# Kernel tuning notes

Hardware: AMD Instinct MI355X
Metric: run time of the kernel (lower is better)

Reference implementation:

```python
import jax, jax.numpy as jnp
import numpy as np

N = 100000
E = 1600000
IN_C = 128
HID = 32
H1 = 4
OUT_C = 32
H2 = 1
NEG_SLOPE = 0.2


def setup_inputs() -> dict:
    key = jax.random.key(0)
    ks = jax.random.split(key, 12)
    g = 0.1  # glorot-ish scale
    return {
        "x": jax.random.normal(ks[0], (N, IN_C), jnp.float32),
        "edge_index": jax.random.randint(ks[1], (2, E), 0, N, jnp.int64),
        "W1": jax.random.normal(ks[2], (IN_C, H1 * HID), jnp.float32) * g,
        "att_src1": jax.random.normal(ks[3], (H1, HID), jnp.float32) * g,
        "att_dst1": jax.random.normal(ks[4], (H1, HID), jnp.float32) * g,
        "b1": jnp.zeros((H1 * HID,), jnp.float32),
        "W2": jax.random.normal(ks[5], (H1 * HID, H2 * OUT_C), jnp.float32) * g,
        "att_src2": jax.random.normal(ks[6], (H2, OUT_C), jnp.float32) * g,
        "att_dst2": jax.random.normal(ks[7], (H2, OUT_C), jnp.float32) * g,
        "b2": jnp.zeros((H2 * OUT_C,), jnp.float32),
    }


def gat_conv(x, src, dst, W, att_src, att_dst, bias, heads, ch):
    n = x.shape[0]
    h = (x @ W).reshape(n, heads, ch)                      # [N,H,C]
    a_src = jnp.sum(h * att_src, axis=-1)                  # [N,H]
    a_dst = jnp.sum(h * att_dst, axis=-1)                  # [N,H]
    e = jax.nn.leaky_relu(a_src[src] + a_dst[dst], NEG_SLOPE)  # [E,H]
    # segment softmax over destination neighborhoods
    m = jax.ops.segment_max(e, dst, num_segments=n)        # [N,H]
    ex = jnp.exp(e - m[dst])
    denom = jax.ops.segment_sum(ex, dst, num_segments=n)   # [N,H]
    alpha = ex / (denom[dst] + 1e-16)                      # [E,H]
    msg = h[src] * alpha[:, :, None]                       # [E,H,C]
    out = jax.ops.segment_sum(msg, dst, num_segments=n)    # [N,H,C]
    return out.reshape(n, heads * ch) + bias


def reference(x, edge_index, W1, att_src1, att_dst1, b1, W2, att_src2, att_dst2, b2):
    # PyG GATConv add_self_loops=True
    loops = jnp.arange(N, dtype=edge_index.dtype)
    src = jnp.concatenate([edge_index[0], loops])
    dst = jnp.concatenate([edge_index[1], loops])
    # dropout is a no-op at inference
    h = gat_conv(x, src, dst, W1, att_src1, att_dst1, b1, H1, HID)
    h = jax.nn.relu(h)
    out = gat_conv(h, src, dst, W2, att_src2, att_dst2, b2, H2, OUT_C)
    return out
```

## Files before the change

### kernel.cpp

```cpp
#include <hip/hip_runtime.h>
#include <hip/hip_bf16.h>


#define NSLOPE 0.2f
#define GSTRIDE 136
#define NB_MAX 400
#define CHUNK 4096
#define CAP 5632

typedef __attribute__((ext_vector_type(8))) short short8;
typedef __attribute__((ext_vector_type(4))) float floatx4;

__device__ __forceinline__ float leaky(float v) { return v > 0.f ? v : NSLOPE * v; }

__device__ __forceinline__ unsigned short f2bf(float f) {
  __hip_bfloat16 b = __float2bfloat16(f);
  return *reinterpret_cast<unsigned short*>(&b);
}
__device__ __forceinline__ float bf2f(unsigned int u) {
  return __uint_as_float(u << 16);
}
__device__ __forceinline__ unsigned int pack2(float a, float b) {
  return (unsigned int)f2bf(a) | ((unsigned int)f2bf(b) << 16);
}

__global__ __launch_bounds__(256) void zero_kernel(int* __restrict__ bincur, int nb) {
  int i = blockIdx.x * 256 + threadIdx.x;
  if (i < nb) bincur[i] = i * CAP;
}

__global__ __launch_bounds__(256) void binA_kernel(const int* __restrict__ ei,
                                                   int* __restrict__ bincur,
                                                   unsigned int* __restrict__ staging,
                                                   int E, int ET, int nb) {
  __shared__ int hist[NB_MAX];
  __shared__ int run[NB_MAX];
  __shared__ int rbase[NB_MAX];
  const int t = threadIdx.x;
  const int base = blockIdx.x * CHUNK;
  for (int i = t; i < nb; i += 256) { hist[i] = 0; run[i] = 0; }
  __syncthreads();
  int se[16], de[16];
#pragma unroll
  for (int j = 0; j < 16; j++) {
    int idx = base + j * 256 + t;
    if (idx < ET) {
      if (idx < E) { se[j] = ei[idx]; de[j] = ei[E + idx]; }
      else         { se[j] = de[j] = idx - E; }
      atomicAdd(&hist[de[j] >> 8], 1);
    } else de[j] = -1;
  }
  __syncthreads();
  for (int i = t; i < nb; i += 256)
    rbase[i] = hist[i] ? atomicAdd(&bincur[i], hist[i]) : 0;
  __syncthreads();
#pragma unroll
  for (int j = 0; j < 16; j++) {
    if (de[j] >= 0) {
      int b = de[j] >> 8;
      int ofs = atomicAdd(&run[b], 1);
      staging[(size_t)rbase[b] + ofs] =
          (unsigned)se[j] | ((unsigned)(de[j] & 255) << 17);
    }
  }
}

__global__ __launch_bounds__(256) void binB_kernel(const unsigned int* __restrict__ staging,
                                                   const int* __restrict__ bincur,
                                                   int* __restrict__ rowbeg,
                                                   int* __restrict__ rowend,
                                                   int* __restrict__ bucket, int n) {
  __shared__ int cnt[256];
  __shared__ int cur[256];
  const int b = blockIdx.x;
  const int t = threadIdx.x;
  const int d0 = b << 8;
  const int nd = min(256, n - d0);
  const int base = b * CAP;
  const int rcnt = bincur[b] - base;
  cnt[t] = 0;
  __syncthreads();
  for (int j = t; j < rcnt; j += 256) {
    unsigned int r = staging[(size_t)base + j];
    atomicAdd(&cnt[r >> 17], 1);
  }
  __syncthreads();
  int v = cnt[t];
  cur[t] = v;
  __syncthreads();
  for (int off = 1; off < 256; off <<= 1) {
    int add = (t >= off) ? cur[t - off] : 0;
    __syncthreads();
    cur[t] += add;
    __syncthreads();
  }
  int start = base + cur[t] - v;
  if (t < nd) { rowbeg[d0 + t] = start; rowend[d0 + t] = start + v; }
  __syncthreads();
  cur[t] = start;
  __syncthreads();
  for (int j = t; j < rcnt; j += 256) {
    unsigned int r = staging[(size_t)base + j];
    int pos = atomicAdd(&cur[r >> 17], 1);
    bucket[pos] = (int)(r & 0x1FFFFu);
  }
}

__global__ __launch_bounds__(256, 2) void gemm1_kernel(const float* __restrict__ x,
                                                       const float* __restrict__ W,
                                                       const float* __restrict__ atts,
                                                       const float* __restrict__ attd,
                                                       unsigned short* __restrict__ h,
                                                       float* __restrict__ asrc,
                                                       float* __restrict__ adst, int n) {
  __shared__ __align__(16) unsigned short xs[128 * GSTRIDE];
  __shared__ __align__(16) unsigned short wt[128 * GSTRIDE];
  __shared__ float att_s[128], att_d[128];
  const int tid = threadIdx.x;
  const int row0 = blockIdx.x * 128;

  if (tid < 128) { att_s[tid] = atts[tid]; att_d[tid] = attd[tid]; }

  const float4* w4 = (const float4*)W;
#pragma unroll
  for (int i = 0; i < 16; i++) {
    int idx = tid + i * 256;
    int k = idx >> 5, n0 = (idx & 31) * 4;
    float4 v = w4[idx];
    float vv[4] = {v.x, v.y, v.z, v.w};
#pragma unroll
    for (int jj = 0; jj < 4; jj++) {
      int j = (jj + tid) & 3;
      wt[(n0 + j) * GSTRIDE + k] = f2bf(vv[j]);
    }
  }

  const float4* x4 = (const float4*)x;
#pragma unroll
  for (int i = 0; i < 16; i++) {
    int idx = tid + i * 256;
    int r = idx >> 5, c4 = idx & 31;
    float4 v = make_float4(0.f, 0.f, 0.f, 0.f);
    if (row0 + r < n) v = x4[(size_t)(row0 + r) * 32 + c4];
    unsigned int* p = (unsigned int*)&xs[r * GSTRIDE + c4 * 4];
    p[0] = pack2(v.x, v.y);
    p[1] = pack2(v.z, v.w);
  }
  __syncthreads();

  const int l = tid & 63;
  const int w = tid >> 6;
  const int mrow = l & 15;
  const int q = l >> 4;
  floatx4 acc[2][8];
#pragma unroll
  for (int mt = 0; mt < 2; mt++)
#pragma unroll
    for (int nt = 0; nt < 8; nt++) acc[mt][nt] = (floatx4){0.f, 0.f, 0.f, 0.f};

#pragma unroll
  for (int ks = 0; ks < 4; ks++) {
    const int k0 = ks * 32 + q * 8;
    short8 a0 = *(const short8*)&xs[(w * 32 + mrow) * GSTRIDE + k0];
    short8 a1 = *(const short8*)&xs[(w * 32 + 16 + mrow) * GSTRIDE + k0];
#pragma unroll
    for (int nt = 0; nt < 8; nt++) {
      short8 b = *(const short8*)&wt[(nt * 16 + mrow) * GSTRIDE + k0];
      acc[0][nt] = __builtin_amdgcn_mfma_f32_16x16x32_bf16(a0, b, acc[0][nt], 0, 0, 0);
      acc[1][nt] = __builtin_amdgcn_mfma_f32_16x16x32_bf16(a1, b, acc[1][nt], 0, 0, 0);
    }
  }
  __syncthreads();

#pragma unroll
  for (int mt = 0; mt < 2; mt++)
#pragma unroll
    for (int nt = 0; nt < 8; nt++)
#pragma unroll
      for (int i = 0; i < 4; i++) {
        int r = w * 32 + mt * 16 + q * 4 + i;
        xs[r * GSTRIDE + nt * 16 + mrow] = f2bf(acc[mt][nt][i]);
      }
  __syncthreads();

#pragma unroll
  for (int i = 0; i < 8; i++) {
    int idx = tid + i * 256;
    int r = idx >> 4, c8 = (idx & 15) * 8;
    if (row0 + r < n) {
      unsigned int* p = (unsigned int*)&xs[r * GSTRIDE + c8];
      uint4 v = make_uint4(p[0], p[1], p[2], p[3]);
      *(uint4*)(h + (size_t)(row0 + r) * 128 + c8) = v;
    }
  }

#pragma unroll
  for (int rr = 0; rr < 2; rr++) {
    int row = (tid >> 2) + rr * 64;
    int head = tid & 3;
    float ss = 0.f, sd = 0.f;
#pragma unroll
    for (int c = 0; c < 32; c++) {
      int cr = (c + tid) & 31;
      float hv = bf2f(xs[row * GSTRIDE + head * 32 + cr]);
      ss += hv * att_s[head * 32 + cr];
      sd += hv * att_d[head * 32 + cr];
    }
    if (row0 + row < n) {
      asrc[(size_t)(row0 + row) * 4 + head] = ss;
      adst[(size_t)(row0 + row) * 4 + head] = sd;
    }
  }
}

__global__ __launch_bounds__(256, 2) void gemm2_kernel(const float* __restrict__ agg1,
                                                       const float* __restrict__ b1,
                                                       const float* __restrict__ W,
                                                       const float* __restrict__ atts,
                                                       const float* __restrict__ attd,
                                                       unsigned short* __restrict__ h2,
                                                       float* __restrict__ asrc,
                                                       float* __restrict__ adst, int n) {
  __shared__ __align__(16) unsigned short xs[128 * GSTRIDE];
  __shared__ __align__(16) unsigned short wt[32 * GSTRIDE];
  __shared__ __align__(16) unsigned short hs[128 * 36];
  __shared__ float att_s[32], att_d[32];
  const int tid = threadIdx.x;
  const int row0 = blockIdx.x * 128;

  if (tid < 32) { att_s[tid] = atts[tid]; att_d[tid] = attd[tid]; }

  const float4* w4 = (const float4*)W;
#pragma unroll
  for (int i = 0; i < 4; i++) {
    int idx = tid + i * 256;
    int k = idx >> 3, n0 = (idx & 7) * 4;
    float4 v = w4[idx];
    float vv[4] = {v.x, v.y, v.z, v.w};
#pragma unroll
    for (int jj = 0; jj < 4; jj++) {
      int j = (jj + tid) & 3;
      wt[(n0 + j) * GSTRIDE + k] = f2bf(vv[j]);
    }
  }

  const float4* a4 = (const float4*)agg1;
#pragma unroll
  for (int i = 0; i < 16; i++) {
    int idx = tid + i * 256;
    int r = idx >> 5, c4 = idx & 31;
    float4 v = make_float4(0.f, 0.f, 0.f, 0.f);
    if (row0 + r < n) {
      float4 a = a4[(size_t)(row0 + r) * 32 + c4];
      float4 b = ((const float4*)b1)[c4];
      v.x = fmaxf(a.x + b.x, 0.f);
      v.y = fmaxf(a.y + b.y, 0.f);
      v.z = fmaxf(a.z + b.z, 0.f);
      v.w = fmaxf(a.w + b.w, 0.f);
    }
    unsigned int* p = (unsigned int*)&xs[r * GSTRIDE + c4 * 4];
    p[0] = pack2(v.x, v.y);
    p[1] = pack2(v.z, v.w);
  }
  __syncthreads();

  const int l = tid & 63;
  const int w = tid >> 6;
  const int mrow = l & 15;
  const int q = l >> 4;
  floatx4 acc[2][2];
#pragma unroll
  for (int mt = 0; mt < 2; mt++)
#pragma unroll
    for (int nt = 0; nt < 2; nt++) acc[mt][nt] = (floatx4){0.f, 0.f, 0.f, 0.f};

#pragma unroll
  for (int ks = 0; ks < 4; ks++) {
    const int k0 = ks * 32 + q * 8;
    short8 a0 = *(const short8*)&xs[(w * 32 + mrow) * GSTRIDE + k0];
    short8 a1 = *(const short8*)&xs[(w * 32 + 16 + mrow) * GSTRIDE + k0];
#pragma unroll
    for (int nt = 0; nt < 2; nt++) {
      short8 b = *(const short8*)&wt[(nt * 16 + mrow) * GSTRIDE + k0];
      acc[0][nt] = __builtin_amdgcn_mfma_f32_16x16x32_bf16(a0, b, acc[0][nt], 0, 0, 0);
      acc[1][nt] = __builtin_amdgcn_mfma_f32_16x16x32_bf16(a1, b, acc[1][nt], 0, 0, 0);
    }
  }

#pragma unroll
  for (int mt = 0; mt < 2; mt++)
#pragma unroll
    for (int nt = 0; nt < 2; nt++)
#pragma unroll
      for (int i = 0; i < 4; i++) {
        int r = w * 32 + mt * 16 + q * 4 + i;
        hs[r * 36 + nt * 16 + mrow] = f2bf(acc[mt][nt][i]);
      }
  __syncthreads();

#pragma unroll
  for (int i = 0; i < 4; i++) {
    int idx = tid + i * 256;
    int r = idx >> 3, c4 = (idx & 7) * 4;
    if (row0 + r < n) {
      unsigned int* p = (unsigned int*)&hs[r * 36 + c4];
      *(uint2*)(h2 + (size_t)(row0 + r) * 32 + c4) = make_uint2(p[0], p[1]);
    }
  }

  if (tid < 128) {
    int row = tid;
    float ss = 0.f, sd = 0.f;
#pragma unroll
    for (int c = 0; c < 32; c++) {
      int cr = (c + tid) & 31;
      float hv = bf2f(hs[row * 36 + cr]);
      ss += hv * att_s[cr];
      sd += hv * att_d[cr];
    }
    if (row0 + row < n) { asrc[row0 + row] = ss; adst[row0 + row] = sd; }
  }
}

__global__ __launch_bounds__(256) void g1_kernel(const int* __restrict__ rowbeg,
                                                 const int* __restrict__ rowend,
                                                 const int* __restrict__ bucket,
                                                 const float* __restrict__ asrc,
                                                 const float* __restrict__ adst,
                                                 const unsigned int* __restrict__ h,
                                                 float* __restrict__ agg, int n) {
  const int lane = threadIdx.x & 63;
  const int g = lane >> 3;
  const int l8 = lane & 7;
  const int head = l8 >> 1;
  const int d = blockIdx.x * 4 + (threadIdx.x >> 6);
  if (d >= n) return;
  const float ad = adst[(size_t)d * 4 + head];
  const int beg = rowbeg[d], end = rowend[d];
  float num[16];
#pragma unroll
  for (int j = 0; j < 16; j++) num[j] = 0.f;
  float den = 0.f;

  int i = beg + g;
  if (i < end) {
    int s = bucket[i];
    for (;;) {
      float a = asrc[(size_t)s * 4 + head];
      const uint4* hp = (const uint4*)(h + (size_t)s * 64 + l8 * 8);
      uint4 h0 = hp[0];
      uint4 h1v = hp[1];
      int i2 = i + 8;
      int s2 = (i2 < end) ? bucket[i2] : 0;
      float w = __expf(leaky(a + ad));
      den += w;
      num[0]  += w * bf2f(h0.x & 0xffffu);  num[1]  += w * bf2f(h0.x >> 16);
      num[2]  += w * bf2f(h0.y & 0xffffu);  num[3]  += w * bf2f(h0.y >> 16);
      num[4]  += w * bf2f(h0.z & 0xffffu);  num[5]  += w * bf2f(h0.z >> 16);
      num[6]  += w * bf2f(h0.w & 0xffffu);  num[7]  += w * bf2f(h0.w >> 16);
      num[8]  += w * bf2f(h1v.x & 0xffffu); num[9]  += w * bf2f(h1v.x >> 16);
      num[10] += w * bf2f(h1v.y & 0xffffu); num[11] += w * bf2f(h1v.y >> 16);
      num[12] += w * bf2f(h1v.z & 0xffffu); num[13] += w * bf2f(h1v.z >> 16);
      num[14] += w * bf2f(h1v.w & 0xffffu); num[15] += w * bf2f(h1v.w >> 16);
      if (i2 >= end) break;
      i = i2; s = s2;
    }
  }
#pragma unroll
  for (int j = 0; j < 16; j++) {
    num[j] += __shfl_xor(num[j], 8, 64);
    num[j] += __shfl_xor(num[j], 16, 64);
    num[j] += __shfl_xor(num[j], 32, 64);
  }
  den += __shfl_xor(den, 8, 64);
  den += __shfl_xor(den, 16, 64);
  den += __shfl_xor(den, 32, 64);
  if (g == 0) {
    float inv = 1.f / (den + 1e-16f);
    float* p = agg + (size_t)d * 128 + l8 * 16;
#pragma unroll
    for (int j = 0; j < 4; j++)
      *(float4*)(p + j * 4) = make_float4(num[j * 4] * inv, num[j * 4 + 1] * inv,
                                          num[j * 4 + 2] * inv, num[j * 4 + 3] * inv);
  }
}

__global__ __launch_bounds__(256) void g2_kernel(const int* __restrict__ rowbeg,
                                                 const int* __restrict__ rowend,
                                                 const int* __restrict__ bucket,
                                                 const float* __restrict__ asrc,
                                                 const float* __restrict__ adst,
                                                 const unsigned int* __restrict__ h2,
                                                 const float* __restrict__ b2,
                                                 float* __restrict__ out, int n) {
  const int lane = threadIdx.x & 63;
  const int g = lane >> 3;
  const int l8 = lane & 7;
  const int d = blockIdx.x * 4 + (threadIdx.x >> 6);
  if (d >= n) return;
  const float ad = adst[d];
  const int beg = rowbeg[d], end = rowend[d];
  float num[4];
#pragma unroll
  for (int j = 0; j < 4; j++) num[j] = 0.f;
  float den = 0.f;

  int i = beg + g;
  if (i < end) {
    int s = bucket[i];
    for (;;) {
      float a = asrc[s];
      uint2 hv = *(const uint2*)(h2 + (size_t)s * 16 + l8 * 2);
      int i2 = i + 8;
      int s2 = (i2 < end) ? bucket[i2] : 0;
      float w = __expf(leaky(a + ad));
      den += w;
      num[0] += w * bf2f(hv.x & 0xffffu); num[1] += w * bf2f(hv.x >> 16);
      num[2] += w * bf2f(hv.y & 0xffffu); num[3] += w * bf2f(hv.y >> 16);
      if (i2 >= end) break;
      i = i2; s = s2;
    }
  }
#pragma unroll
  for (int j = 0; j < 4; j++) {
    num[j] += __shfl_xor(num[j], 8, 64);
    num[j] += __shfl_xor(num[j], 16, 64);
    num[j] += __shfl_xor(num[j], 32, 64);
  }
  den += __shfl_xor(den, 8, 64);
  den += __shfl_xor(den, 16, 64);
  den += __shfl_xor(den, 32, 64);
  if (g == 0) {
    float inv = 1.f / (den + 1e-16f);
    float4 bv = ((const float4*)b2)[l8];
    *(float4*)(out + (size_t)d * 32 + l8 * 4) =
        make_float4(num[0] * inv + bv.x, num[1] * inv + bv.y,
                    num[2] * inv + bv.z, num[3] * inv + bv.w);
  }
}

extern "C" void kernel_launch(void* const* d_in, const int* in_sizes, int n_in,
                              void* d_out, int out_size, void* d_ws, size_t ws_size,
                              hipStream_t stream) {
  const float* x = (const float*)d_in[0];
  const int* ei = (const int*)d_in[1];
  const float* W1 = (const float*)d_in[2];
  const float* atts1 = (const float*)d_in[3];
  const float* attd1 = (const float*)d_in[4];
  const float* b1 = (const float*)d_in[5];
  const float* W2 = (const float*)d_in[6];
  const float* atts2 = (const float*)d_in[7];
  const float* attd2 = (const float*)d_in[8];
  const float* b2 = (const float*)d_in[9];
  float* out = (float*)d_out;

  const int N = in_sizes[0] / 128;
  const int E = in_sizes[1] / 2;
  const int ET = E + N;
  const int NB = (N + 255) >> 8;
  const int NCH = (ET + CHUNK - 1) / CHUNK;

  float* wsf = (float*)d_ws;
  float* agg1 = wsf;
  float* asrc1 = agg1 + (size_t)N * 128;
  float* adst1 = asrc1 + (size_t)N * 4;
  float* asrc2 = adst1 + (size_t)N * 4;
  float* adst2 = asrc2 + (size_t)N;
  unsigned short* h1 = (unsigned short*)(adst2 + (size_t)N);
  unsigned short* h2 = h1;
  int* rowbeg = (int*)(h1 + (size_t)N * 128);
  int* rowend = rowbeg + N;
  int* bucket = rowend + N;
  int* bincur = bucket + (size_t)NB * CAP;
  unsigned int* staging = (unsigned int*)(bincur + NB);

  zero_kernel<<<(NB + 255) / 256, 256, 0, stream>>>(bincur, NB);
  gemm1_kernel<<<(N + 127) / 128, 256, 0, stream>>>(x, W1, atts1, attd1, h1, asrc1, adst1, N);
  binA_kernel<<<NCH, 256, 0, stream>>>(ei, bincur, staging, E, ET, NB);
  binB_kernel<<<NB, 256, 0, stream>>>(staging, bincur, rowbeg, rowend, bucket, N);
  g1_kernel<<<(N + 3) / 4, 256, 0, stream>>>(rowbeg, rowend, bucket, asrc1, adst1,
                                             (const unsigned int*)h1, agg1, N);
  gemm2_kernel<<<(N + 127) / 128, 256, 0, stream>>>(agg1, b1, W2, atts2, attd2, h2, asrc2, adst2, N);
  g2_kernel<<<(N + 3) / 4, 256, 0, stream>>>(rowbeg, rowend, bucket, asrc2, adst2,
                                             (const unsigned int*)h2, b2, out, N);
}
```

Measured before the change: 306.2 us.

## Fuse binning into GEMM1 launch and CSR build into aggregation kernels via LDS

GEMM1 and the edge-binning pass now run in one launch, with blocks split by role, so the two independent phases can overlap. The second binning pass (local sort per 256-node bin) is folded into both aggregation kernels: each 1024-thread block rebuilds its bin's CSR in LDS, so the global bucket, rowbeg and rowend arrays are no longer written and reread. The layer-1 aggregate is stored as bf16 instead of fp32, halving that intermediate's traffic into GEMM2. In exchange the local sort is done twice, occupancy may drop from large LDS and block sizes, and the extra bf16 rounding slightly reduces precision.

```diff
diff --git a/kernel.cpp b/kernel.cpp
--- a/kernel.cpp
+++ b/kernel.cpp
@@ -29,191 +29,254 @@
   if (i < nb) bincur[i] = i * CAP;
 }
 
-__global__ __launch_bounds__(256) void binA_kernel(const int* __restrict__ ei,
-                                                   int* __restrict__ bincur,
-                                                   unsigned int* __restrict__ staging,
-                                                   int E, int ET, int nb) {
-  __shared__ int hist[NB_MAX];
-  __shared__ int run[NB_MAX];
-  __shared__ int rbase[NB_MAX];
-  const int t = threadIdx.x;
-  const int base = blockIdx.x * CHUNK;
-  for (int i = t; i < nb; i += 256) { hist[i] = 0; run[i] = 0; }
-  __syncthreads();
-  int se[16], de[16];
-#pragma unroll
-  for (int j = 0; j < 16; j++) {
-    int idx = base + j * 256 + t;
-    if (idx < ET) {
-      if (idx < E) { se[j] = ei[idx]; de[j] = ei[E + idx]; }
-      else         { se[j] = de[j] = idx - E; }
-      atomicAdd(&hist[de[j] >> 8], 1);
-    } else de[j] = -1;
-  }
-  __syncthreads();
-  for (int i = t; i < nb; i += 256)
-    rbase[i] = hist[i] ? atomicAdd(&bincur[i], hist[i]) : 0;
-  __syncthreads();
-#pragma unroll
-  for (int j = 0; j < 16; j++) {
-    if (de[j] >= 0) {
-      int b = de[j] >> 8;
-      int ofs = atomicAdd(&run[b], 1);
-      staging[(size_t)rbase[b] + ofs] =
-          (unsigned)se[j] | ((unsigned)(de[j] & 255) << 17);
-    }
-  }
-}
-
-__global__ __launch_bounds__(256) void binB_kernel(const unsigned int* __restrict__ staging,
-                                                   const int* __restrict__ bincur,
-                                                   int* __restrict__ rowbeg,
-                                                   int* __restrict__ rowend,
-                                                   int* __restrict__ bucket, int n) {
-  __shared__ int cnt[256];
-  __shared__ int cur[256];
+__global__ __launch_bounds__(256, 2) void fused1_kernel(
+    const float* __restrict__ x, const float* __restrict__ W,
+    const float* __restrict__ atts, const float* __restrict__ attd,
+    unsigned short* __restrict__ h, float* __restrict__ asrc, float* __restrict__ adst,
+    int n, int g1blocks,
+    const int* __restrict__ ei, int* __restrict__ bincur,
+    unsigned int* __restrict__ staging, int E, int ET, int nb) {
+  __shared__ __align__(16) unsigned char smem[70656];
+  const int tid = threadIdx.x;
+
+  if (blockIdx.x < g1blocks) {
+    unsigned short* xs = (unsigned short*)smem;
+    unsigned short* wt = (unsigned short*)(smem + 34816);
+    float* att_s = (float*)(smem + 69632);
+    float* att_d = (float*)(smem + 70144);
+    const int row0 = blockIdx.x * 128;
+
+    if (tid < 128) { att_s[tid] = atts[tid]; att_d[tid] = attd[tid]; }
+
+    const float4* w4 = (const float4*)W;
+#pragma unroll
+    for (int i = 0; i < 16; i++) {
+      int idx = tid + i * 256;
+      int k = idx >> 5, n0 = (idx & 31) * 4;
+      float4 v = w4[idx];
+      float vv[4] = {v.x, v.y, v.z, v.w};
+#pragma unroll
+      for (int jj = 0; jj < 4; jj++) {
+        int j = (jj + tid) & 3;
+        wt[(n0 + j) * GSTRIDE + k] = f2bf(vv[j]);
+      }
+    }
+
+    const float4* x4 = (const float4*)x;
+#pragma unroll
+    for (int i = 0; i < 16; i++) {
+      int idx = tid + i * 256;
+      int r = idx >> 5, c4 = idx & 31;
+      float4 v = make_float4(0.f, 0.f, 0.f, 0.f);
+      if (row0 + r < n) v = x4[(size_t)(row0 + r) * 32 + c4];
+      unsigned int* p = (unsigned int*)&xs[r * GSTRIDE + c4 * 4];
+      p[0] = pack2(v.x, v.y);
+      p[1] = pack2(v.z, v.w);
+    }
+    __syncthreads();
+
+    const int l = tid & 63;
+    const int w = tid >> 6;
+    const int mrow = l & 15;
+    const int q = l >> 4;
+    floatx4 acc[2][8];
+#pragma unroll
+    for (int mt = 0; mt < 2; mt++)
+#pragma unroll
+      for (int nt = 0; nt < 8; nt++) acc[mt][nt] = (floatx4){0.f, 0.f, 0.f, 0.f};
+
+#pragma unroll
+    for (int ks = 0; ks < 4; ks++) {
+      const int k0 = ks * 32 + q * 8;
+      short8 a0 = *(const short8*)&xs[(w * 32 + mrow) * GSTRIDE + k0];
+      short8 a1 = *(const short8*)&xs[(w * 32 + 16 + mrow) * GSTRIDE + k0];
+#pragma unroll
+      for (int nt = 0; nt < 8; nt++) {
+        short8 b = *(const short8*)&wt[(nt * 16 + mrow) * GSTRIDE + k0];
+        acc[0][nt] = __builtin_amdgcn_mfma_f32_16x16x32_bf16(a0, b, acc[0][nt], 0, 0, 0);
+        acc[1][nt] = __builtin_amdgcn_mfma_f32_16x16x32_bf16(a1, b, acc[1][nt], 0, 0, 0);
+      }
+    }
+    __syncthreads();
+
+#pragma unroll
+    for (int mt = 0; mt < 2; mt++)
+#pragma unroll
+      for (int nt = 0; nt < 8; nt++)
+#pragma unroll
+        for (int i = 0; i < 4; i++) {
+          int r = w * 32 + mt * 16 + q * 4 + i;
+          xs[r * GSTRIDE + nt * 16 + mrow] = f2bf(acc[mt][nt][i]);
+        }
+    __syncthreads();
+
+#pragma unroll
+    for (int i = 0; i < 8; i++) {
+      int idx = tid + i * 256;
+      int r = idx >> 4, c8 = (idx & 15) * 8;
+      if (row0 + r < n) {
+        unsigned int* p = (unsigned int*)&xs[r * GSTRIDE + c8];
+        uint4 v = make_uint4(p[0], p[1], p[2], p[3]);
+        *(uint4*)(h + (size_t)(row0 + r) * 128 + c8) = v;
+      }
+    }
+
+#pragma unroll
+    for (int rr = 0; rr < 2; rr++) {
+      int row = (tid >> 2) + rr * 64;
+      int head = tid & 3;
+      float ss = 0.f, sd = 0.f;
+#pragma unroll
+      for (int c = 0; c < 32; c++) {
+        int cr = (c + tid) & 31;
+        float hv = bf2f(xs[row * GSTRIDE + head * 32 + cr]);
+        ss += hv * att_s[head * 32 + cr];
+        sd += hv * att_d[head * 32 + cr];
+      }
+      if (row0 + row < n) {
+        asrc[(size_t)(row0 + row) * 4 + head] = ss;
+        adst[(size_t)(row0 + row) * 4 + head] = sd;
+      }
+    }
+  } else {
+    int* hist  = (int*)smem;
+    int* run   = (int*)(smem + 1600);
+    int* rbase = (int*)(smem + 3200);
+    const int base = (blockIdx.x - g1blocks) * CHUNK;
+    for (int i = tid; i < nb; i += 256) { hist[i] = 0; run[i] = 0; }
+    __syncthreads();
+    int se[16], de[16];
+#pragma unroll
+    for (int j = 0; j < 16; j++) {
+      int idx = base + j * 256 + tid;
+      if (idx < ET) {
+        if (idx < E) { se[j] = ei[idx]; de[j] = ei[E + idx]; }
+        else         { se[j] = de[j] = idx - E; }
+        atomicAdd(&hist[de[j] >> 8], 1);
+      } else de[j] = -1;
+    }
+    __syncthreads();
+    for (int i = tid; i < nb; i += 256)
+      rbase[i] = hist[i] ? atomicAdd(&bincur[i], hist[i]) : 0;
+    __syncthreads();
+#pragma unroll
+    for (int j = 0; j < 16; j++) {
+      if (de[j] >= 0) {
+        int b = de[j] >> 8;
+        int ofs = atomicAdd(&run[b], 1);
+        staging[(size_t)rbase[b] + ofs] =
+            (unsigned)se[j] | ((unsigned)(de[j] & 255) << 17);
+      }
+    }
+  }
+}
+
+__global__ __launch_bounds__(1024, 8) void g1_kernel(const unsigned int* __restrict__ staging,
+                                                     const int* __restrict__ bincur,
+                                                     const float* __restrict__ asrc,
+                                                     const float* __restrict__ adst,
+                                                     const unsigned int* __restrict__ h,
+                                                     unsigned short* __restrict__ agg,
+                                                     int n) {
+  __shared__ int lbucket[CAP];
+  __shared__ int cnt[256], cur[256], rbeg[256];
   const int b = blockIdx.x;
   const int t = threadIdx.x;
   const int d0 = b << 8;
   const int nd = min(256, n - d0);
   const int base = b * CAP;
   const int rcnt = bincur[b] - base;
-  cnt[t] = 0;
-  __syncthreads();
-  for (int j = t; j < rcnt; j += 256) {
-    unsigned int r = staging[(size_t)base + j];
-    atomicAdd(&cnt[r >> 17], 1);
-  }
-  __syncthreads();
-  int v = cnt[t];
-  cur[t] = v;
+
+  if (t < 256) cnt[t] = 0;
+  __syncthreads();
+  for (int j = t; j < rcnt; j += 1024)
+    atomicAdd(&cnt[staging[(size_t)base + j] >> 17], 1);
+  __syncthreads();
+  int v = 0;
+  if (t < 256) { v = cnt[t]; cur[t] = v; }
   __syncthreads();
   for (int off = 1; off < 256; off <<= 1) {
-    int add = (t >= off) ? cur[t - off] : 0;
-    __syncthreads();
-    cur[t] += add;
-    __syncthreads();
-  }
-  int start = base + cur[t] - v;
-  if (t < nd) { rowbeg[d0 + t] = start; rowend[d0 + t] = start + v; }
-  __syncthreads();
-  cur[t] = start;
-  __syncthreads();
-  for (int j = t; j < rcnt; j += 256) {
+    int add = (t < 256 && t >= off) ? cur[t - off] : 0;
+    __syncthreads();
+    if (t < 256) cur[t] += add;
+    __syncthreads();
+  }
+  if (t < 256) { rbeg[t] = cur[t] - v; cur[t] = cur[t] - v; }
+  __syncthreads();
+  for (int j = t; j < rcnt; j += 1024) {
     unsigned int r = staging[(size_t)base + j];
     int pos = atomicAdd(&cur[r >> 17], 1);
-    bucket[pos] = (int)(r & 0x1FFFFu);
-  }
-}
-
-__global__ __launch_bounds__(256, 2) void gemm1_kernel(const float* __restrict__ x,
-                                                       const float* __restrict__ W,
-                                                       const float* __restrict__ atts,
-                                                       const float* __restrict__ attd,
-                                                       unsigned short* __restrict__ h,
-                                                       float* __restrict__ asrc,
-                                                       float* __restrict__ adst, int n) {
-  __shared__ __align__(16) unsigned short xs[128 * GSTRIDE];
-  __shared__ __align__(16) unsigned short wt[128 * GSTRIDE];
-  __shared__ float att_s[128], att_d[128];
-  const int tid = threadIdx.x;
-  const int row0 = blockIdx.x * 128;
-
-  if (tid < 128) { att_s[tid] = atts[tid]; att_d[tid] = attd[tid]; }
-
-  const float4* w4 = (const float4*)W;
-#pragma unroll
-  for (int i = 0; i < 16; i++) {
-    int idx = tid + i * 256;
-    int k = idx >> 5, n0 = (idx & 31) * 4;
-    float4 v = w4[idx];
-    float vv[4] = {v.x, v.y, v.z, v.w};
-#pragma unroll
-    for (int jj = 0; jj < 4; jj++) {
-      int j = (jj + tid) & 3;
-      wt[(n0 + j) * GSTRIDE + k] = f2bf(vv[j]);
-    }
-  }
-
-  const float4* x4 = (const float4*)x;
-#pragma unroll
-  for (int i = 0; i < 16; i++) {
-    int idx = tid + i * 256;
-    int r = idx >> 5, c4 = idx & 31;
-    float4 v = make_float4(0.f, 0.f, 0.f, 0.f);
-    if (row0 + r < n) v = x4[(size_t)(row0 + r) * 32 + c4];
-    unsigned int* p = (unsigned int*)&xs[r * GSTRIDE + c4 * 4];
-    p[0] = pack2(v.x, v.y);
-    p[1] = pack2(v.z, v.w);
-  }
-  __syncthreads();
-
-  const int l = tid & 63;
-  const int w = tid >> 6;
-  const int mrow = l & 15;
-  const int q = l >> 4;
-  floatx4 acc[2][8];
-#pragma unroll
-  for (int mt = 0; mt < 2; mt++)
-#pragma unroll
-    for (int nt = 0; nt < 8; nt++) acc[mt][nt] = (floatx4){0.f, 0.f, 0.f, 0.f};
-
-#pragma unroll
-  for (int ks = 0; ks < 4; ks++) {
-    const int k0 = ks * 32 + q * 8;
-    short8 a0 = *(const short8*)&xs[(w * 32 + mrow) * GSTRIDE + k0];
-    short8 a1 = *(const short8*)&xs[(w * 32 + 16 + mrow) * GSTRIDE + k0];
-#pragma unroll
-    for (int nt = 0; nt < 8; nt++) {
-      short8 b = *(const short8*)&wt[(nt * 16 + mrow) * GSTRIDE + k0];
-      acc[0][nt] = __builtin_amdgcn_mfma_f32_16x16x32_bf16(a0, b, acc[0][nt], 0, 0, 0);
-      acc[1][nt] = __builtin_amdgcn_mfma_f32_16x16x32_bf16(a1, b, acc[1][nt], 0, 0, 0);
-    }
-  }
-  __syncthreads();
-
-#pragma unroll
-  for (int mt = 0; mt < 2; mt++)
-#pragma unroll
-    for (int nt = 0; nt < 8; nt++)
-#pragma unroll
-      for (int i = 0; i < 4; i++) {
-        int r = w * 32 + mt * 16 + q * 4 + i;
-        xs[r * GSTRIDE + nt * 16 + mrow] = f2bf(acc[mt][nt][i]);
-      }
-  __syncthreads();
-
-#pragma unroll
-  for (int i = 0; i < 8; i++) {
-    int idx = tid + i * 256;
-    int r = idx >> 4, c8 = (idx & 15) * 8;
-    if (row0 + r < n) {
-      unsigned int* p = (unsigned int*)&xs[r * GSTRIDE + c8];
-      uint4 v = make_uint4(p[0], p[1], p[2], p[3]);
-      *(uint4*)(h + (size_t)(row0 + r) * 128 + c8) = v;
-    }
-  }
-
-#pragma unroll
-  for (int rr = 0; rr < 2; rr++) {
-    int row = (tid >> 2) + rr * 64;
-    int head = tid & 3;
-    float ss = 0.f, sd = 0.f;
-#pragma unroll
-    for (int c = 0; c < 32; c++) {
-      int cr = (c + tid) & 31;
-      float hv = bf2f(xs[row * GSTRIDE + head * 32 + cr]);
-      ss += hv * att_s[head * 32 + cr];
-      sd += hv * att_d[head * 32 + cr];
-    }
-    if (row0 + row < n) {
-      asrc[(size_t)(row0 + row) * 4 + head] = ss;
-      adst[(size_t)(row0 + row) * 4 + head] = sd;
-    }
-  }
-}
-
-__global__ __launch_bounds__(256, 2) void gemm2_kernel(const float* __restrict__ agg1,
+    lbucket[pos] = (int)(r & 0x1FFFFu);
+  }
+  __syncthreads();
+
+  const int wv = t >> 6;
+  const int lane = t & 63;
+  const int g = lane >> 3;
+  const int l8 = lane & 7;
+  const int head = l8 >> 1;
+  for (int dd = wv; dd < nd; dd += 16) {
+    const int d = d0 + dd;
+    const float ad = adst[(size_t)d * 4 + head];
+    const int beg = rbeg[dd];
+    const int end = beg + cnt[dd];
+    float num[16];
+#pragma unroll
+    for (int j = 0; j < 16; j++) num[j] = 0.f;
+    float den = 0.f;
+
+    int i = beg + g;
+    if (i < end) {
+      int s = lbucket[i];
+      for (;;) {
+        float a = asrc[(size_t)s * 4 + head];
+        const uint4* hp = (const uint4*)(h + (size_t)s * 64 + l8 * 8);
+        uint4 h0 = hp[0];
+        uint4 h1v = hp[1];
+        int i2 = i + 8;
+        int s2 = (i2 < end) ? lbucket[i2] : 0;
+        float w = __expf(leaky(a + ad));
+        den += w;
+        num[0]  += w * bf2f(h0.x & 0xffffu);  num[1]  += w * bf2f(h0.x >> 16);
+        num[2]  += w * bf2f(h0.y & 0xffffu);  num[3]  += w * bf2f(h0.y >> 16);
+        num[4]  += w * bf2f(h0.z & 0xffffu);  num[5]  += w * bf2f(h0.z >> 16);
+        num[6]  += w * bf2f(h0.w & 0xffffu);  num[7]  += w * bf2f(h0.w >> 16);
+        num[8]  += w * bf2f(h1v.x & 0xffffu); num[9]  += w * bf2f(h1v.x >> 16);
+        num[10] += w * bf2f(h1v.y & 0xffffu); num[11] += w * bf2f(h1v.y >> 16);
+        num[12] += w * bf2f(h1v.z & 0xffffu); num[13] += w * bf2f(h1v.z >> 16);
+        num[14] += w * bf2f(h1v.w & 0xffffu); num[15] += w * bf2f(h1v.w >> 16);
+        if (i2 >= end) break;
+        i = i2; s = s2;
+      }
+    }
+#pragma unroll
+    for (int j = 0; j < 16; j++) {
+      num[j] += __shfl_xor(num[j], 8, 64);
+      num[j] += __shfl_xor(num[j], 16, 64);
+      num[j] += __shfl_xor(num[j], 32, 64);
+    }
+    den += __shfl_xor(den, 8, 64);
+    den += __shfl_xor(den, 16, 64);
+    den += __shfl_xor(den, 32, 64);
+    if (g == 0) {
+      float inv = 1.f / (den + 1e-16f);
+      unsigned short* p = agg + (size_t)d * 128 + l8 * 16;
+      uint4 o0, o1;
+      o0.x = pack2(num[0] * inv, num[1] * inv);
+      o0.y = pack2(num[2] * inv, num[3] * inv);
+      o0.z = pack2(num[4] * inv, num[5] * inv);
+      o0.w = pack2(num[6] * inv, num[7] * inv);
+      o1.x = pack2(num[8] * inv, num[9] * inv);
+      o1.y = pack2(num[10] * inv, num[11] * inv);
+      o1.z = pack2(num[12] * inv, num[13] * inv);
+      o1.w = pack2(num[14] * inv, num[15] * inv);
+      *(uint4*)p = o0;
+      *(uint4*)(p + 8) = o1;
+    }
+  }
+}
+
+__global__ __launch_bounds__(256, 2) void gemm2_kernel(const unsigned short* __restrict__ agg1,
                                                        const float* __restrict__ b1,
                                                        const float* __restrict__ W,
                                                        const float* __restrict__ atts,
@@ -244,23 +307,21 @@
     }
   }
 
-  const float4* a4 = (const float4*)agg1;
-#pragma unroll
-  for (int i = 0; i < 16; i++) {
+  const uint4* a4 = (const uint4*)agg1;
+#pragma unroll
+  for (int i = 0; i < 8; i++) {
     int idx = tid + i * 256;
-    int r = idx >> 5, c4 = idx & 31;
-    float4 v = make_float4(0.f, 0.f, 0.f, 0.f);
-    if (row0 + r < n) {
-      float4 a = a4[(size_t)(row0 + r) * 32 + c4];
-      float4 b = ((const float4*)b1)[c4];
-      v.x = fmaxf(a.x + b.x, 0.f);
-      v.y = fmaxf(a.y + b.y, 0.f);
-      v.z = fmaxf(a.z + b.z, 0.f);
-      v.w = fmaxf(a.w + b.w, 0.f);
-    }
-    unsigned int* p = (unsigned int*)&xs[r * GSTRIDE + c4 * 4];
-    p[0] = pack2(v.x, v.y);
-    p[1] = pack2(v.z, v.w);
+    int r = idx >> 4, c8 = (idx & 15) * 8;
+    uint4 v = make_uint4(0, 0, 0, 0);
+    if (row0 + r < n) v = a4[(size_t)(row0 + r) * 16 + (idx & 15)];
+    unsigned int* p = (unsigned int*)&xs[r * GSTRIDE + c8];
+    unsigned int vw[4] = {v.x, v.y, v.z, v.w};
+#pragma unroll
+    for (int j = 0; j < 4; j++) {
+      float lo = fmaxf(bf2f(vw[j] & 0xffffu) + b1[c8 + j * 2], 0.f);
+      float hi = fmaxf(bf2f(vw[j] >> 16) + b1[c8 + j * 2 + 1], 0.f);
+      p[j] = pack2(lo, hi);
+    }
   }
   __syncthreads();
 
@@ -322,120 +383,91 @@
   }
 }
 
-__global__ __launch_bounds__(256) void g1_kernel(const int* __restrict__ rowbeg,
-                                                 const int* __restrict__ rowend,
-                                                 const int* __restrict__ bucket,
-                                                 const float* __restrict__ asrc,
-                                                 const float* __restrict__ adst,
-                                                 const unsigned int* __restrict__ h,
-                                                 float* __restrict__ agg, int n) {
-  const int lane = threadIdx.x & 63;
+__global__ __launch_bounds__(1024, 8) void g2_kernel(const unsigned int* __restrict__ staging,
+                                                     const int* __restrict__ bincur,
+                                                     const float* __restrict__ asrc,
+                                                     const float* __restrict__ adst,
+                                                     const unsigned int* __restrict__ h2,
+                                                     const float* __restrict__ b2,
+                                                     float* __restrict__ out, int n) {
+  __shared__ int lbucket[CAP];
+  __shared__ int cnt[256], cur[256], rbeg[256];
+  const int b = blockIdx.x;
+  const int t = threadIdx.x;
+  const int d0 = b << 8;
+  const int nd = min(256, n - d0);
+  const int base = b * CAP;
+  const int rcnt = bincur[b] - base;
+
+  if (t < 256) cnt[t] = 0;
+  __syncthreads();
+  for (int j = t; j < rcnt; j += 1024)
+    atomicAdd(&cnt[staging[(size_t)base + j] >> 17], 1);
+  __syncthreads();
+  int v = 0;
+  if (t < 256) { v = cnt[t]; cur[t] = v; }
+  __syncthreads();
+  for (int off = 1; off < 256; off <<= 1) {
+    int add = (t < 256 && t >= off) ? cur[t - off] : 0;
+    __syncthreads();
+    if (t < 256) cur[t] += add;
+    __syncthreads();
+  }
+  if (t < 256) { rbeg[t] = cur[t] - v; cur[t] = cur[t] - v; }
+  __syncthreads();
+  for (int j = t; j < rcnt; j += 1024) {
+    unsigned int r = staging[(size_t)base + j];
+    int pos = atomicAdd(&cur[r >> 17], 1);
+    lbucket[pos] = (int)(r & 0x1FFFFu);
+  }
+  __syncthreads();
+
+  const int wv = t >> 6;
+  const int lane = t & 63;
   const int g = lane >> 3;
   const int l8 = lane & 7;
-  const int head = l8 >> 1;
-  const int d = blockIdx.x * 4 + (threadIdx.x >> 6);
-  if (d >= n) return;
-  const float ad = adst[(size_t)d * 4 + head];
-  const int beg = rowbeg[d], end = rowend[d];
-  float num[16];
-#pragma unroll
-  for (int j = 0; j < 16; j++) num[j] = 0.f;
-  float den = 0.f;
-
-  int i = beg + g;
-  if (i < end) {
-    int s = bucket[i];
-    for (;;) {
-      float a = asrc[(size_t)s * 4 + head];
-      const uint4* hp = (const uint4*)(h + (size_t)s * 64 + l8 * 8);
-      uint4 h0 = hp[0];
-      uint4 h1v = hp[1];
-      int i2 = i + 8;
-      int s2 = (i2 < end) ? bucket[i2] : 0;
-      float w = __expf(leaky(a + ad));
-      den += w;
-      num[0]  += w * bf2f(h0.x & 0xffffu);  num[1]  += w * bf2f(h0.x >> 16);
-      num[2]  += w * bf2f(h0.y & 0xffffu);  num[3]  += w * bf2f(h0.y >> 16);
-      num[4]  += w * bf2f(h0.z & 0xffffu);  num[5]  += w * bf2f(h0.z >> 16);
-      num[6]  += w * bf2f(h0.w & 0xffffu);  num[7]  += w * bf2f(h0.w >> 16);
-      num[8]  += w * bf2f(h1v.x & 0xffffu); num[9]  += w * bf2f(h1v.x >> 16);
-      num[10] += w * bf2f(h1v.y & 0xffffu); num[11] += w * bf2f(h1v.y >> 16);
-      num[12] += w * bf2f(h1v.z & 0xffffu); num[13] += w * bf2f(h1v.z >> 16);
-      num[14] += w * bf2f(h1v.w & 0xffffu); num[15] += w * bf2f(h1v.w >> 16);
-      if (i2 >= end) break;
-      i = i2; s = s2;
-    }
-  }
-#pragma unroll
-  for (int j = 0; j < 16; j++) {
-    num[j] += __shfl_xor(num[j], 8, 64);
-    num[j] += __shfl_xor(num[j], 16, 64);
-    num[j] += __shfl_xor(num[j], 32, 64);
-  }
-  den += __shfl_xor(den, 8, 64);
-  den += __shfl_xor(den, 16, 64);
-  den += __shfl_xor(den, 32, 64);
-  if (g == 0) {
-    float inv = 1.f / (den + 1e-16f);
-    float* p = agg + (size_t)d * 128 + l8 * 16;
-#pragma unroll
-    for (int j = 0; j < 4; j++)
-      *(float4*)(p + j * 4) = make_float4(num[j * 4] * inv, num[j * 4 + 1] * inv,
-                                          num[j * 4 + 2] * inv, num[j * 4 + 3] * inv);
-  }
-}
-
-__global__ __launch_bounds__(256) void g2_kernel(const int* __restrict__ rowbeg,
-                                                 const int* __restrict__ rowend,
-                                                 const int* __restrict__ bucket,
-                                                 const float* __restrict__ asrc,
-                                                 const float* __restrict__ adst,
-                                                 const unsigned int* __restrict__ h2,
-                                                 const float* __restrict__ b2,
-                                                 float* __restrict__ out, int n) {
-  const int lane = threadIdx.x & 63;
-  const int g = lane >> 3;
-  const int l8 = lane & 7;
-  const int d = blockIdx.x * 4 + (threadIdx.x >> 6);
-  if (d >= n) return;
-  const float ad = adst[d];
-  const int beg = rowbeg[d], end = rowend[d];
-  float num[4];
-#pragma unroll
-  for (int j = 0; j < 4; j++) num[j] = 0.f;
-  float den = 0.f;
-
-  int i = beg + g;
-  if (i < end) {
-    int s = bucket[i];
-    for (;;) {
-      float a = asrc[s];
-      uint2 hv = *(const uint2*)(h2 + (size_t)s * 16 + l8 * 2);
-      int i2 = i + 8;
-      int s2 = (i2 < end) ? bucket[i2] : 0;
-      float w = __expf(leaky(a + ad));
-      den += w;
-      num[0] += w * bf2f(hv.x & 0xffffu); num[1] += w * bf2f(hv.x >> 16);
-      num[2] += w * bf2f(hv.y & 0xffffu); num[3] += w * bf2f(hv.y >> 16);
-      if (i2 >= end) break;
-      i = i2; s = s2;
-    }
-  }
-#pragma unroll
-  for (int j = 0; j < 4; j++) {
-    num[j] += __shfl_xor(num[j], 8, 64);
-    num[j] += __shfl_xor(num[j], 16, 64);
-    num[j] += __shfl_xor(num[j], 32, 64);
-  }
-  den += __shfl_xor(den, 8, 64);
-  den += __shfl_xor(den, 16, 64);
-  den += __shfl_xor(den, 32, 64);
-  if (g == 0) {
-    float inv = 1.f / (den + 1e-16f);
-    float4 bv = ((const float4*)b2)[l8];
-    *(float4*)(out + (size_t)d * 32 + l8 * 4) =
-        make_float4(num[0] * inv + bv.x, num[1] * inv + bv.y,
-                    num[2] * inv + bv.z, num[3] * inv + bv.w);
+  for (int dd = wv; dd < nd; dd += 16) {
+    const int d = d0 + dd;
+    const float ad = adst[d];
+    const int beg = rbeg[dd];
+    const int end = beg + cnt[dd];
+    float num[4];
+#pragma unroll
+    for (int j = 0; j < 4; j++) num[j] = 0.f;
+    float den = 0.f;
+
+    int i = beg + g;
+    if (i < end) {
+      int s = lbucket[i];
+      for (;;) {
+        float a = asrc[s];
+        uint2 hv = *(const uint2*)(h2 + (size_t)s * 16 + l8 * 2);
+        int i2 = i + 8;
+        int s2 = (i2 < end) ? lbucket[i2] : 0;
+        float w = __expf(leaky(a + ad));
+        den += w;
+        num[0] += w * bf2f(hv.x & 0xffffu); num[1] += w * bf2f(hv.x >> 16);
+        num[2] += w * bf2f(hv.y & 0xffffu); num[3] += w * bf2f(hv.y >> 16);
+        if (i2 >= end) break;
+        i = i2; s = s2;
+      }
+    }
+#pragma unroll
+    for (int j = 0; j < 4; j++) {
+      num[j] += __shfl_xor(num[j], 8, 64);
+      num[j] += __shfl_xor(num[j], 16, 64);
+      num[j] += __shfl_xor(num[j], 32, 64);
+    }
+    den += __shfl_xor(den, 8, 64);
+    den += __shfl_xor(den, 16, 64);
+    den += __shfl_xor(den, 32, 64);
+    if (g == 0) {
+      float inv = 1.f / (den + 1e-16f);
+      float4 bb = ((const float4*)b2)[l8];
+      *(float4*)(out + (size_t)d * 32 + l8 * 4) =
+          make_float4(num[0] * inv + bb.x, num[1] * inv + bb.y,
+                      num[2] * inv + bb.z, num[3] * inv + bb.w);
+    }
   }
 }
 
@@ -459,28 +491,26 @@
   const int ET = E + N;
   const int NB = (N + 255) >> 8;
   const int NCH = (ET + CHUNK - 1) / CHUNK;
+  const int G1B = (N + 127) / 128;
 
   float* wsf = (float*)d_ws;
-  float* agg1 = wsf;
-  float* asrc1 = agg1 + (size_t)N * 128;
+  float* asrc1 = wsf;
   float* adst1 = asrc1 + (size_t)N * 4;
   float* asrc2 = adst1 + (size_t)N * 4;
   float* adst2 = asrc2 + (size_t)N;
-  unsigned short* h1 = (unsigned short*)(adst2 + (size_t)N);
+  unsigned short* agg1 = (unsigned short*)(adst2 + (size_t)N);
+  unsigned short* h1 = agg1 + (size_t)N * 128;
   unsigned short* h2 = h1;
-  int* rowbeg = (int*)(h1 + (size_t)N * 128);
-  int* rowend = rowbeg + N;
-  int* bucket = rowend + N;
-  int* bincur = bucket + (size_t)NB * CAP;
-  unsigned int* staging = (unsigned int*)(bincur + NB);
+  unsigned int* staging = (unsigned int*)(h1 + (size_t)N * 128);
+  int* bincur = (int*)(staging + (size_t)NB * CAP);
 
   zero_kernel<<<(NB + 255) / 256, 256, 0, stream>>>(bincur, NB);
-  gemm1_kernel<<<(N + 127) / 128, 256, 0, stream>>>(x, W1, atts1, attd1, h1, asrc1, adst1, N);
-  binA_kernel<<<NCH, 256, 0, stream>>>(ei, bincur, staging, E, ET, NB);
-  binB_kernel<<<NB, 256, 0, stream>>>(staging, bincur, rowbeg, rowend, bucket, N);
-  g1_kernel<<<(N + 3) / 4, 256, 0, stream>>>(rowbeg, rowend, bucket, asrc1, adst1,
-                                             (const unsigned int*)h1, agg1, N);
-  gemm2_kernel<<<(N + 127) / 128, 256, 0, stream>>>(agg1, b1, W2, atts2, attd2, h2, asrc2, adst2, N);
-  g2_kernel<<<(N + 3) / 4, 256, 0, stream>>>(rowbeg, rowend, bucket, asrc2, adst2,
-                                             (const unsigned int*)h2, b2, out, N);
-}
+  fused1_kernel<<<G1B + NCH, 256, 0, stream>>>(x, W1, atts1, attd1, h1, asrc1, adst1,
+                                               N, G1B, ei, bincur, staging, E, ET, NB);
+  g1_kernel<<<NB, 1024, 0, stream>>>(staging, bincur, asrc1, adst1,
+                                     (const unsigned int*)h1, agg1, N);
+  gemm2_kernel<<<(N + 127) / 128, 256, 0, stream>>>(agg1, b1, W2, atts2, attd2,
+                                                    h2, asrc2, adst2, N);
+  g2_kernel<<<NB, 1024, 0, stream>>>(staging, bincur, asrc2, adst2,
+                                     (const unsigned int*)h2, b2, out, N);
+}
```

Result: faster. 289.2 us (-5.6%).
